# Performance work log

Measured on AMD Instinct MI355X. Metric: run time of the kernel, lower is better.

The kernel has to match this reference:

```python
import jax, jax.numpy as jnp
import numpy as np

B, S = 1, 2048
H, KV, D = 32, 8, 128          # query heads, kv heads, head_size
G = H // KV                     # num_queries_per_kv (GQA group size)
SCALE = 1.0 / float(np.sqrt(D))


def setup_inputs() -> dict:
    key = jax.random.key(0)
    k1, k2, k3 = jax.random.split(key, 3)
    slopes = jnp.asarray(2.0 ** (-8.0 * np.arange(1, H + 1) / H), dtype=jnp.float32)
    return {
        "query": jax.random.normal(k1, (B, S, H * D), dtype=jnp.float32),
        "key": jax.random.normal(k2, (B, S, KV * D), dtype=jnp.float32),
        "value": jax.random.normal(k3, (B, S, KV * D), dtype=jnp.float32),
        "alibi_slopes": slopes,
    }


def reference(query, key, value, alibi_slopes):
    b, s, _ = query.shape
    # [B,S,H*D] -> [B,KV,G,S,D] (GQA unflatten of query heads into kv groups)
    q = query.reshape(b, s, KV, G, D).transpose(0, 2, 3, 1, 4)
    k = key.reshape(b, s, KV, D).transpose(0, 2, 1, 3)      # [B,KV,S,D]
    v = value.reshape(b, s, KV, D).transpose(0, 2, 1, 3)    # [B,KV,S,D]

    # _make_alibi_bias: bias[i,j] = (j - i) * slope_h, then unflatten heads to (KV, G)
    pos = jnp.arange(s)
    rel = (pos[None, :] - pos[:, None]).astype(query.dtype)         # [S,S]
    bias = alibi_slopes[:, None, None] * rel                        # [H,S,S]
    causal = jnp.where(pos[None, :] > pos[:, None], -jnp.inf, 0.0).astype(query.dtype)
    bias = (bias + causal).reshape(KV, G, s, s)                     # [KV,G,S,S]

    # scaled QK^T + bias, softmax, AV (non-fused prompt_attention path)
    scores = jnp.einsum('bkgsd,bktd->bkgst', q * SCALE, k) + bias   # [B,KV,G,S,S]
    probs = jax.nn.softmax(scores, axis=-1)
    out = jnp.einsum('bkgst,bktd->bkgsd', probs, v)                 # [B,KV,G,S,D]
    # flatten (KV,G) -> H and back to [B,S,H*D]
    return out.transpose(0, 3, 1, 2, 4).reshape(b, s, H * D)
```

## Files before the change

kernel.cpp:

```cpp
#include <hip/hip_runtime.h>
#include <hip/hip_bf16.h>

#define S_LEN 2048
#define NHEADS 32
#define NKV 8
#define HD 128
#define QK_SCALE 0.08838834764831845f
#define LOG2E 1.4426950408889634f
#define QK_SCALE2 (QK_SCALE * LOG2E)
#define DTHR 11.5416f

#define BQ 64
#define BK 32
#define NQT (S_LEN / BQ)
#define QSTR (NHEADS * HD)
#define KSTR (NKV * HD)

#define K_STRIDE 136
#define VT_STRIDE 40
#define P_STRIDE 40

typedef __attribute__((ext_vector_type(8))) short bf16x8;
typedef __attribute__((ext_vector_type(4))) float f32x4;
typedef __attribute__((ext_vector_type(4))) unsigned u32x4;
typedef __attribute__((ext_vector_type(2))) unsigned u32x2;

__device__ inline unsigned cvt_pk_bf16(float lo, float hi) {
    unsigned r;
    asm("v_cvt_pk_bf16_f32 %0, %1, %2" : "=v"(r) : "v"(lo), "v"(hi));
    return r;
}
__device__ inline bf16x8 as_bf16x8(u32x4 v) {
    union { u32x4 u; bf16x8 b; } c; c.u = v; return c.b;
}

__global__ __launch_bounds__(256) void prep_k(const float* __restrict__ K,
                                              short* __restrict__ Kbf) {
    int g = blockIdx.x * 256 + threadIdx.x;
    int chunk = g & 15, kvh = (g >> 4) & 7, s = g >> 7;
    const float* in = K + (size_t)s * KSTR + kvh * HD + chunk * 8;
    f32x4 a = *(const f32x4*)in;
    f32x4 b = *(const f32x4*)(in + 4);
    u32x4 t;
    t[0] = cvt_pk_bf16(a[0], a[1]); t[1] = cvt_pk_bf16(a[2], a[3]);
    t[2] = cvt_pk_bf16(b[0], b[1]); t[3] = cvt_pk_bf16(b[2], b[3]);
    *(u32x4*)(Kbf + ((size_t)kvh * S_LEN + s) * HD + chunk * 8) = t;
}

__global__ __launch_bounds__(256) void prep_v(const float* __restrict__ V,
                                              short* __restrict__ Vtb) {
    __shared__ short Ts[64][72];
    int b = blockIdx.x;
    int sb = b & 31, db = (b >> 5) & 1, kvh = b >> 6;
    int t = threadIdx.x, r = t >> 2, c0 = (t & 3) * 16;

    const float* in = V + (size_t)(sb * 64 + r) * KSTR + kvh * HD + db * 64 + c0;
    f32x4 a0 = *(const f32x4*)in,        a1 = *(const f32x4*)(in + 4);
    f32x4 a2 = *(const f32x4*)(in + 8),  a3 = *(const f32x4*)(in + 12);
    u32x4 t0;
    t0[0] = cvt_pk_bf16(a0[0], a0[1]); t0[1] = cvt_pk_bf16(a0[2], a0[3]);
    t0[2] = cvt_pk_bf16(a1[0], a1[1]); t0[3] = cvt_pk_bf16(a1[2], a1[3]);
    *(u32x4*)&Ts[r][c0] = t0;
    t0[0] = cvt_pk_bf16(a2[0], a2[1]); t0[1] = cvt_pk_bf16(a2[2], a2[3]);
    t0[2] = cvt_pk_bf16(a3[0], a3[1]); t0[3] = cvt_pk_bf16(a3[2], a3[3]);
    *(u32x4*)&Ts[r][c0 + 8] = t0;
    __syncthreads();

    alignas(16) short tmp[16];
    #pragma unroll
    for (int j = 0; j < 16; ++j) tmp[j] = Ts[c0 + j][r];
    short* dst = Vtb + ((size_t)(kvh * HD + db * 64 + r)) * S_LEN + sb * 64 + c0;
    *(u32x4*)dst       = *(u32x4*)&tmp[0];
    *(u32x4*)(dst + 8) = *(u32x4*)&tmp[8];
}

__global__ __launch_bounds__(256) void attn_fwd(
    const float* __restrict__ Q, const short* __restrict__ Kbf,
    const short* __restrict__ Vtb, const float* __restrict__ SL,
    float* __restrict__ O)
{
    const int bx   = blockIdx.x;
    const int h    = bx & (NHEADS - 1);
    const int qt   = (NQT - 1) - (bx >> 5);
    const int kvh  = h >> 2;
    const float slope  = SL[h];
    const float slope2 = slope * LOG2E;

    const int tid  = threadIdx.x;
    const int lane = tid & 63;
    const int w    = tid >> 6;
    const int l16  = lane & 15;
    const int lq   = lane >> 4;

    __shared__ short Ks[2][BK * K_STRIDE];
    __shared__ short VTs[2][HD * VT_STRIDE];
    __shared__ short Ps[4][16 * P_STRIDE];

    const int qrow0 = qt * BQ + w * 16;
    const int q     = qrow0 + l16;

    bf16x8 qf[4];
    {
        const float* qp = Q + (size_t)q * QSTR + h * HD + lq * 8;
        #pragma unroll
        for (int d0 = 0; d0 < 4; ++d0) {
            f32x4 a = *(const f32x4*)(qp + d0 * 32);
            f32x4 b = *(const f32x4*)(qp + d0 * 32 + 4);
            u32x4 t;
            t[0] = cvt_pk_bf16(a[0] * QK_SCALE2, a[1] * QK_SCALE2);
            t[1] = cvt_pk_bf16(a[2] * QK_SCALE2, a[3] * QK_SCALE2);
            t[2] = cvt_pk_bf16(b[0] * QK_SCALE2, b[1] * QK_SCALE2);
            t[3] = cvt_pk_bf16(b[2] * QK_SCALE2, b[3] * QK_SCALE2);
            qf[d0] = as_bf16x8(t);
        }
    }
    bf16x8 onesf;
    #pragma unroll
    for (int j = 0; j < 8; ++j) onesf[j] = (short)0x3f80;

    f32x4 acc[8];
    #pragma unroll
    for (int t = 0; t < 8; ++t) acc[t] = (f32x4){0.f, 0.f, 0.f, 0.f};
    f32x4 sums = (f32x4){0.f, 0.f, 0.f, 0.f};
    float m_ = -1e30f;

    const int kv_end = qt * BQ + BQ;
    int kb_start = 0;
    {
        float th = (float)(qt * BQ) - 31.0f - 45.0f / slope;
        int t = (int)floorf(th);
        kb_start = (t < 0) ? 0 : (((t >> 5) + 1) << 5);
    }

    const int sr  = tid >> 4, scc = tid & 15;
    const int vd  = tid & 127, vrb = (tid >> 7) * 8;
    const short* Kst = Kbf + (size_t)kvh * S_LEN * HD + scc * 8;
    const short* Vst = Vtb + (size_t)(kvh * HD + vd) * S_LEN;

    u32x4 kreg[2], vreg[2];

    auto load_regs = [&](int kb) {
        #pragma unroll
        for (int s = 0; s < 2; ++s)
            kreg[s] = *(const u32x4*)(Kst + (size_t)(kb + sr + s * 16) * HD);
        #pragma unroll
        for (int s = 0; s < 2; ++s)
            vreg[s] = *(const u32x4*)(Vst + kb + vrb + s * 16);
    };

    auto store_tile = [&](int b) {
        #pragma unroll
        for (int s = 0; s < 2; ++s)
            *(u32x4*)&Ks[b][(sr + s * 16) * K_STRIDE + scc * 8] = kreg[s];
        #pragma unroll
        for (int s = 0; s < 2; ++s)
            *(u32x4*)&VTs[b][vd * VT_STRIDE + vrb + s * 16] = vreg[s];
    };

    load_regs(kb_start);
    store_tile(0);
    int cur = 0;

    for (int kb = kb_start; kb < kv_end; kb += BK) {
        asm volatile("s_waitcnt lgkmcnt(0)\n\ts_barrier" ::: "memory");

        const bool has_next = (kb + BK) < kv_end;
        if (has_next) load_regs(kb + BK);

        const bool live = (kb <= qrow0 + 15) &&
                          (slope * (float)(qrow0 - kb - 31) < 45.0f);
        if (live) {
            const short* Kc = &Ks[cur][0];
            const short* Vc = &VTs[cur][0];

            f32x4 sc0 = (f32x4){0.f,0.f,0.f,0.f};
            f32x4 sc1 = (f32x4){0.f,0.f,0.f,0.f};
            #pragma unroll
            for (int d0 = 0; d0 < 4; ++d0) {
                bf16x8 kf0 = *(const bf16x8*)&Kc[l16 * K_STRIDE + d0 * 32 + lq * 8];
                bf16x8 kf1 = *(const bf16x8*)&Kc[(16 + l16) * K_STRIDE + d0 * 32 + lq * 8];
                sc0 = __builtin_amdgcn_mfma_f32_16x16x32_bf16(kf0, qf[d0], sc0, 0, 0, 0);
                sc1 = __builtin_amdgcn_mfma_f32_16x16x32_bf16(kf1, qf[d0], sc1, 0, 0, 0);
            }

            const int kq0 = kb + 4 * lq - q;
            float s[8];
            #pragma unroll
            for (int i = 0; i < 4; ++i) {
                int d0i = kq0 + i, d1i = kq0 + 16 + i;
                float b0 = __builtin_fmaf(slope2, (float)d0i, sc0[i]);
                float b1 = __builtin_fmaf(slope2, (float)d1i, sc1[i]);
                s[i]     = (d0i > 0) ? -1e30f : b0;
                s[i + 4] = (d1i > 0) ? -1e30f : b1;
            }

            float lm = fmaxf(fmaxf(fmaxf(s[0], s[1]), fmaxf(s[2], s[3])),
                             fmaxf(fmaxf(s[4], s[5]), fmaxf(s[6], s[7])));
            if (__any(lm > m_ + DTHR)) {
                float rm = lm;
                rm = fmaxf(rm, __shfl_xor(rm, 16));
                rm = fmaxf(rm, __shfl_xor(rm, 32));
                if (rm > m_ + DTHR) {
                    float alpha = exp2f(m_ - rm);
                    m_ = rm;
                    sums[0] *= alpha; sums[1] *= alpha;
                    sums[2] *= alpha; sums[3] *= alpha;
                    #pragma unroll
                    for (int t = 0; t < 8; ++t) {
                        acc[t][0] *= alpha; acc[t][1] *= alpha;
                        acc[t][2] *= alpha; acc[t][3] *= alpha;
                    }
                }
            }

            float p[8];
            #pragma unroll
            for (int j = 0; j < 8; ++j) p[j] = exp2f(s[j] - m_);

            u32x2 pa, pb;
            pa[0] = cvt_pk_bf16(p[0], p[1]); pa[1] = cvt_pk_bf16(p[2], p[3]);
            pb[0] = cvt_pk_bf16(p[4], p[5]); pb[1] = cvt_pk_bf16(p[6], p[7]);

            short* PsW = &Ps[w][0];
            *(u32x2*)&PsW[l16 * P_STRIDE + 4 * lq]      = pa;
            *(u32x2*)&PsW[l16 * P_STRIDE + 16 + 4 * lq] = pb;
            asm volatile("s_waitcnt lgkmcnt(0)" ::: "memory");
            bf16x8 pf = *(const bf16x8*)&PsW[l16 * P_STRIDE + lq * 8];

            sums = __builtin_amdgcn_mfma_f32_16x16x32_bf16(onesf, pf, sums, 0, 0, 0);

            #pragma unroll
            for (int nt = 0; nt < 8; ++nt) {
                bf16x8 vf = *(const bf16x8*)&Vc[(nt * 16 + l16) * VT_STRIDE + lq * 8];
                acc[nt] = __builtin_amdgcn_mfma_f32_16x16x32_bf16(vf, pf, acc[nt], 0, 0, 0);
            }
        }

        if (has_next) store_tile(cur ^ 1);
        cur ^= 1;
    }

    {
        float rl = 1.0f / sums[0];
        float* op = O + (size_t)q * QSTR + h * HD + 4 * lq;
        #pragma unroll
        for (int nt = 0; nt < 8; ++nt) {
            f32x4 o = acc[nt];
            o[0] *= rl; o[1] *= rl; o[2] *= rl; o[3] *= rl;
            *(f32x4*)(op + nt * 16) = o;
        }
    }
}

extern "C" void kernel_launch(void* const* d_in, const int* in_sizes, int n_in,
                              void* d_out, int out_size, void* d_ws, size_t ws_size,
                              hipStream_t stream) {
    const float* Q  = (const float*)d_in[0];
    const float* K  = (const float*)d_in[1];
    const float* V  = (const float*)d_in[2];
    const float* SL = (const float*)d_in[3];
    float* O = (float*)d_out;

    short* Kbf = (short*)d_ws;
    short* Vtb = (short*)d_ws + (size_t)NKV * S_LEN * HD;

    prep_k<<<dim3(1024), dim3(256), 0, stream>>>(K, Kbf);
    prep_v<<<dim3(512),  dim3(256), 0, stream>>>(V, Vtb);
    attn_fwd<<<dim3(NQT * NHEADS), dim3(256), 0, stream>>>(Q, Kbf, Vtb, SL, O);
}
```

Measured before the change: 90.64 us.

## Deepen K/V prefetch to two tiles ahead with ping-pong register slots

Restructures the KV loop into a two-step unrolled ping-pong pipeline. Two register slot sets hold the global loads for tiles t+1 and t+2 while tile t is computed from shared memory. Each shared store happens right after the barrier and before compute, rather than at the end of the iteration. The goal is to hide more global-memory latency behind MFMA work. The cost is about 32 extra VGPRs for the second slot, which may reduce occupancy.

```diff
diff --git a/kernel.cpp b/kernel.cpp
--- a/kernel.cpp
+++ b/kernel.cpp
@@ -131,113 +131,122 @@
         int t = (int)floorf(th);
         kb_start = (t < 0) ? 0 : (((t >> 5) + 1) << 5);
     }
+    const int Ntiles = (kv_end - kb_start) >> 5;
 
     const int sr  = tid >> 4, scc = tid & 15;
     const int vd  = tid & 127, vrb = (tid >> 7) * 8;
     const short* Kst = Kbf + (size_t)kvh * S_LEN * HD + scc * 8;
     const short* Vst = Vtb + (size_t)(kvh * HD + vd) * S_LEN;
 
-    u32x4 kreg[2], vreg[2];
-
-    auto load_regs = [&](int kb) {
-        #pragma unroll
-        for (int s = 0; s < 2; ++s)
-            kreg[s] = *(const u32x4*)(Kst + (size_t)(kb + sr + s * 16) * HD);
-        #pragma unroll
-        for (int s = 0; s < 2; ++s)
-            vreg[s] = *(const u32x4*)(Vst + kb + vrb + s * 16);
+    u32x4 kA[2], vA[2], kB[2], vB[2];
+
+    auto load_slot = [&](u32x4 (&kk)[2], u32x4 (&vv)[2], int kb) {
+        #pragma unroll
+        for (int s = 0; s < 2; ++s)
+            kk[s] = *(const u32x4*)(Kst + (size_t)(kb + sr + s * 16) * HD);
+        #pragma unroll
+        for (int s = 0; s < 2; ++s)
+            vv[s] = *(const u32x4*)(Vst + kb + vrb + s * 16);
     };
-
-    auto store_tile = [&](int b) {
-        #pragma unroll
-        for (int s = 0; s < 2; ++s)
-            *(u32x4*)&Ks[b][(sr + s * 16) * K_STRIDE + scc * 8] = kreg[s];
-        #pragma unroll
-        for (int s = 0; s < 2; ++s)
-            *(u32x4*)&VTs[b][vd * VT_STRIDE + vrb + s * 16] = vreg[s];
+    auto store_slot = [&](int b, u32x4 (&kk)[2], u32x4 (&vv)[2]) {
+        #pragma unroll
+        for (int s = 0; s < 2; ++s)
+            *(u32x4*)&Ks[b][(sr + s * 16) * K_STRIDE + scc * 8] = kk[s];
+        #pragma unroll
+        for (int s = 0; s < 2; ++s)
+            *(u32x4*)&VTs[b][vd * VT_STRIDE + vrb + s * 16] = vv[s];
     };
 
-    load_regs(kb_start);
-    store_tile(0);
-    int cur = 0;
-
-    for (int kb = kb_start; kb < kv_end; kb += BK) {
-        asm volatile("s_waitcnt lgkmcnt(0)\n\ts_barrier" ::: "memory");
-
-        const bool has_next = (kb + BK) < kv_end;
-        if (has_next) load_regs(kb + BK);
-
+    auto compute_tile = [&](int kb, int cb) {
         const bool live = (kb <= qrow0 + 15) &&
                           (slope * (float)(qrow0 - kb - 31) < 45.0f);
-        if (live) {
-            const short* Kc = &Ks[cur][0];
-            const short* Vc = &VTs[cur][0];
-
-            f32x4 sc0 = (f32x4){0.f,0.f,0.f,0.f};
-            f32x4 sc1 = (f32x4){0.f,0.f,0.f,0.f};
-            #pragma unroll
-            for (int d0 = 0; d0 < 4; ++d0) {
-                bf16x8 kf0 = *(const bf16x8*)&Kc[l16 * K_STRIDE + d0 * 32 + lq * 8];
-                bf16x8 kf1 = *(const bf16x8*)&Kc[(16 + l16) * K_STRIDE + d0 * 32 + lq * 8];
-                sc0 = __builtin_amdgcn_mfma_f32_16x16x32_bf16(kf0, qf[d0], sc0, 0, 0, 0);
-                sc1 = __builtin_amdgcn_mfma_f32_16x16x32_bf16(kf1, qf[d0], sc1, 0, 0, 0);
-            }
-
-            const int kq0 = kb + 4 * lq - q;
-            float s[8];
-            #pragma unroll
-            for (int i = 0; i < 4; ++i) {
-                int d0i = kq0 + i, d1i = kq0 + 16 + i;
-                float b0 = __builtin_fmaf(slope2, (float)d0i, sc0[i]);
-                float b1 = __builtin_fmaf(slope2, (float)d1i, sc1[i]);
-                s[i]     = (d0i > 0) ? -1e30f : b0;
-                s[i + 4] = (d1i > 0) ? -1e30f : b1;
-            }
-
-            float lm = fmaxf(fmaxf(fmaxf(s[0], s[1]), fmaxf(s[2], s[3])),
-                             fmaxf(fmaxf(s[4], s[5]), fmaxf(s[6], s[7])));
-            if (__any(lm > m_ + DTHR)) {
-                float rm = lm;
-                rm = fmaxf(rm, __shfl_xor(rm, 16));
-                rm = fmaxf(rm, __shfl_xor(rm, 32));
-                if (rm > m_ + DTHR) {
-                    float alpha = exp2f(m_ - rm);
-                    m_ = rm;
-                    sums[0] *= alpha; sums[1] *= alpha;
-                    sums[2] *= alpha; sums[3] *= alpha;
-                    #pragma unroll
-                    for (int t = 0; t < 8; ++t) {
-                        acc[t][0] *= alpha; acc[t][1] *= alpha;
-                        acc[t][2] *= alpha; acc[t][3] *= alpha;
-                    }
+        if (!live) return;
+        const short* Kc = &Ks[cb][0];
+        const short* Vc = &VTs[cb][0];
+
+        f32x4 sc0 = (f32x4){0.f,0.f,0.f,0.f};
+        f32x4 sc1 = (f32x4){0.f,0.f,0.f,0.f};
+        #pragma unroll
+        for (int d0 = 0; d0 < 4; ++d0) {
+            bf16x8 kf0 = *(const bf16x8*)&Kc[l16 * K_STRIDE + d0 * 32 + lq * 8];
+            bf16x8 kf1 = *(const bf16x8*)&Kc[(16 + l16) * K_STRIDE + d0 * 32 + lq * 8];
+            sc0 = __builtin_amdgcn_mfma_f32_16x16x32_bf16(kf0, qf[d0], sc0, 0, 0, 0);
+            sc1 = __builtin_amdgcn_mfma_f32_16x16x32_bf16(kf1, qf[d0], sc1, 0, 0, 0);
+        }
+
+        const int kq0 = kb + 4 * lq - q;
+        float s[8];
+        #pragma unroll
+        for (int i = 0; i < 4; ++i) {
+            int d0i = kq0 + i, d1i = kq0 + 16 + i;
+            float b0 = __builtin_fmaf(slope2, (float)d0i, sc0[i]);
+            float b1 = __builtin_fmaf(slope2, (float)d1i, sc1[i]);
+            s[i]     = (d0i > 0) ? -1e30f : b0;
+            s[i + 4] = (d1i > 0) ? -1e30f : b1;
+        }
+
+        float lm = fmaxf(fmaxf(fmaxf(s[0], s[1]), fmaxf(s[2], s[3])),
+                         fmaxf(fmaxf(s[4], s[5]), fmaxf(s[6], s[7])));
+        if (__any(lm > m_ + DTHR)) {
+            float rm = lm;
+            rm = fmaxf(rm, __shfl_xor(rm, 16));
+            rm = fmaxf(rm, __shfl_xor(rm, 32));
+            if (rm > m_ + DTHR) {
+                float alpha = exp2f(m_ - rm);
+                m_ = rm;
+                sums[0] *= alpha; sums[1] *= alpha;
+                sums[2] *= alpha; sums[3] *= alpha;
+                #pragma unroll
+                for (int t = 0; t < 8; ++t) {
+                    acc[t][0] *= alpha; acc[t][1] *= alpha;
+                    acc[t][2] *= alpha; acc[t][3] *= alpha;
                 }
             }
-
-            float p[8];
-            #pragma unroll
-            for (int j = 0; j < 8; ++j) p[j] = exp2f(s[j] - m_);
-
-            u32x2 pa, pb;
-            pa[0] = cvt_pk_bf16(p[0], p[1]); pa[1] = cvt_pk_bf16(p[2], p[3]);
-            pb[0] = cvt_pk_bf16(p[4], p[5]); pb[1] = cvt_pk_bf16(p[6], p[7]);
-
-            short* PsW = &Ps[w][0];
-            *(u32x2*)&PsW[l16 * P_STRIDE + 4 * lq]      = pa;
-            *(u32x2*)&PsW[l16 * P_STRIDE + 16 + 4 * lq] = pb;
-            asm volatile("s_waitcnt lgkmcnt(0)" ::: "memory");
-            bf16x8 pf = *(const bf16x8*)&PsW[l16 * P_STRIDE + lq * 8];
-
-            sums = __builtin_amdgcn_mfma_f32_16x16x32_bf16(onesf, pf, sums, 0, 0, 0);
-
-            #pragma unroll
-            for (int nt = 0; nt < 8; ++nt) {
-                bf16x8 vf = *(const bf16x8*)&Vc[(nt * 16 + l16) * VT_STRIDE + lq * 8];
-                acc[nt] = __builtin_amdgcn_mfma_f32_16x16x32_bf16(vf, pf, acc[nt], 0, 0, 0);
-            }
-        }
-
-        if (has_next) store_tile(cur ^ 1);
-        cur ^= 1;
+        }
+
+        float p[8];
+        #pragma unroll
+        for (int j = 0; j < 8; ++j) p[j] = exp2f(s[j] - m_);
+
+        u32x2 pa, pb;
+        pa[0] = cvt_pk_bf16(p[0], p[1]); pa[1] = cvt_pk_bf16(p[2], p[3]);
+        pb[0] = cvt_pk_bf16(p[4], p[5]); pb[1] = cvt_pk_bf16(p[6], p[7]);
+
+        short* PsW = &Ps[w][0];
+        *(u32x2*)&PsW[l16 * P_STRIDE + 4 * lq]      = pa;
+        *(u32x2*)&PsW[l16 * P_STRIDE + 16 + 4 * lq] = pb;
+        asm volatile("s_waitcnt lgkmcnt(0)" ::: "memory");
+        bf16x8 pf = *(const bf16x8*)&PsW[l16 * P_STRIDE + lq * 8];
+
+        sums = __builtin_amdgcn_mfma_f32_16x16x32_bf16(onesf, pf, sums, 0, 0, 0);
+
+        #pragma unroll
+        for (int nt = 0; nt < 8; ++nt) {
+            bf16x8 vf = *(const bf16x8*)&Vc[(nt * 16 + l16) * VT_STRIDE + lq * 8];
+            acc[nt] = __builtin_amdgcn_mfma_f32_16x16x32_bf16(vf, pf, acc[nt], 0, 0, 0);
+        }
+    };
+
+    load_slot(kA, vA, kb_start);
+    store_slot(0, kA, vA);
+    if (Ntiles > 1) load_slot(kB, vB, kb_start + 32);
+    if (Ntiles > 2) load_slot(kA, vA, kb_start + 64);
+
+    int t = 0;
+    for (; t + 2 <= Ntiles; t += 2) {
+        asm volatile("s_waitcnt lgkmcnt(0)\n\ts_barrier" ::: "memory");
+        store_slot(1, kB, vB);
+        if (t + 3 < Ntiles) load_slot(kB, vB, kb_start + (t + 3) * 32);
+        compute_tile(kb_start + t * 32, 0);
+
+        asm volatile("s_waitcnt lgkmcnt(0)\n\ts_barrier" ::: "memory");
+        if (t + 2 < Ntiles) store_slot(0, kA, vA);
+        if (t + 4 < Ntiles) load_slot(kA, vA, kb_start + (t + 4) * 32);
+        compute_tile(kb_start + (t + 1) * 32, 1);
+    }
+    if (t < Ntiles) {
+        asm volatile("s_waitcnt lgkmcnt(0)\n\ts_barrier" ::: "memory");
+        compute_tile(kb_start + t * 32, 0);
     }
 
     {
```

Result: slower. 105.4 us, median of 2 (+16.3%).

## Double query rows per wave to reuse K/V LDS tiles across two sub-tiles

Applied to the files above, without the earlier changes.

Raises the query tile from 64 to 128 rows so each wave handles two 16-row sub-tiles (A and B), each with its own softmax state and accumulators. K and V fragments read from shared memory now feed MFMAs for both sub-tiles, and each K/V tile is staged once for twice as many queries. This halves the grid and roughly doubles accumulator register pressure, which may lower occupancy. It also coarsens the load balance across causal tiles.

```diff
diff --git a/kernel.cpp b/kernel.cpp
--- a/kernel.cpp
+++ b/kernel.cpp
@@ -10,7 +10,7 @@
 #define QK_SCALE2 (QK_SCALE * LOG2E)
 #define DTHR 11.5416f
 
-#define BQ 64
+#define BQ 128
 #define BK 32
 #define NQT (S_LEN / BQ)
 #define QSTR (NHEADS * HD)
@@ -94,14 +94,16 @@
 
     __shared__ short Ks[2][BK * K_STRIDE];
     __shared__ short VTs[2][HD * VT_STRIDE];
-    __shared__ short Ps[4][16 * P_STRIDE];
-
-    const int qrow0 = qt * BQ + w * 16;
-    const int q     = qrow0 + l16;
-
-    bf16x8 qf[4];
-    {
-        const float* qp = Q + (size_t)q * QSTR + h * HD + lq * 8;
+    __shared__ short Ps[4][32 * P_STRIDE];
+
+    const int qrow0 = qt * BQ + w * 32;
+    const int qA    = qrow0 + l16;
+    const int qB    = qA + 16;
+
+    bf16x8 qfA[4], qfB[4];
+    #pragma unroll
+    for (int st = 0; st < 2; ++st) {
+        const float* qp = Q + (size_t)(st ? qB : qA) * QSTR + h * HD + lq * 8;
         #pragma unroll
         for (int d0 = 0; d0 < 4; ++d0) {
             f32x4 a = *(const f32x4*)(qp + d0 * 32);
@@ -111,18 +113,21 @@
             t[1] = cvt_pk_bf16(a[2] * QK_SCALE2, a[3] * QK_SCALE2);
             t[2] = cvt_pk_bf16(b[0] * QK_SCALE2, b[1] * QK_SCALE2);
             t[3] = cvt_pk_bf16(b[2] * QK_SCALE2, b[3] * QK_SCALE2);
-            qf[d0] = as_bf16x8(t);
+            if (st) qfB[d0] = as_bf16x8(t); else qfA[d0] = as_bf16x8(t);
         }
     }
     bf16x8 onesf;
     #pragma unroll
     for (int j = 0; j < 8; ++j) onesf[j] = (short)0x3f80;
 
-    f32x4 acc[8];
+    f32x4 accA[8], accB[8];
     #pragma unroll
-    for (int t = 0; t < 8; ++t) acc[t] = (f32x4){0.f, 0.f, 0.f, 0.f};
-    f32x4 sums = (f32x4){0.f, 0.f, 0.f, 0.f};
-    float m_ = -1e30f;
+    for (int t = 0; t < 8; ++t) {
+        accA[t] = (f32x4){0.f, 0.f, 0.f, 0.f};
+        accB[t] = (f32x4){0.f, 0.f, 0.f, 0.f};
+    }
+    f32x4 sumsA = (f32x4){0.f,0.f,0.f,0.f}, sumsB = (f32x4){0.f,0.f,0.f,0.f};
+    float mA = -1e30f, mB = -1e30f;
 
     const int kv_end = qt * BQ + BQ;
     int kb_start = 0;
@@ -147,7 +152,6 @@
         for (int s = 0; s < 2; ++s)
             vreg[s] = *(const u32x4*)(Vst + kb + vrb + s * 16);
     };
-
     auto store_tile = [&](int b) {
         #pragma unroll
         for (int s = 0; s < 2; ++s)
@@ -167,72 +171,126 @@
         const bool has_next = (kb + BK) < kv_end;
         if (has_next) load_regs(kb + BK);
 
-        const bool live = (kb <= qrow0 + 15) &&
-                          (slope * (float)(qrow0 - kb - 31) < 45.0f);
-        if (live) {
+        const bool liveA = (kb <= qrow0 + 15) &&
+                           (slope * (float)(qrow0 - kb - 31) < 45.0f);
+        const bool liveB = (kb <= qrow0 + 31) &&
+                           (slope * (float)(qrow0 + 16 - kb - 31) < 45.0f);
+
+        if (liveA || liveB) {
             const short* Kc = &Ks[cur][0];
             const short* Vc = &VTs[cur][0];
 
-            f32x4 sc0 = (f32x4){0.f,0.f,0.f,0.f};
-            f32x4 sc1 = (f32x4){0.f,0.f,0.f,0.f};
+            f32x4 sA0 = (f32x4){0.f,0.f,0.f,0.f}, sA1 = (f32x4){0.f,0.f,0.f,0.f};
+            f32x4 sB0 = (f32x4){0.f,0.f,0.f,0.f}, sB1 = (f32x4){0.f,0.f,0.f,0.f};
             #pragma unroll
             for (int d0 = 0; d0 < 4; ++d0) {
                 bf16x8 kf0 = *(const bf16x8*)&Kc[l16 * K_STRIDE + d0 * 32 + lq * 8];
                 bf16x8 kf1 = *(const bf16x8*)&Kc[(16 + l16) * K_STRIDE + d0 * 32 + lq * 8];
-                sc0 = __builtin_amdgcn_mfma_f32_16x16x32_bf16(kf0, qf[d0], sc0, 0, 0, 0);
-                sc1 = __builtin_amdgcn_mfma_f32_16x16x32_bf16(kf1, qf[d0], sc1, 0, 0, 0);
+                if (liveA) {
+                    sA0 = __builtin_amdgcn_mfma_f32_16x16x32_bf16(kf0, qfA[d0], sA0, 0, 0, 0);
+                    sA1 = __builtin_amdgcn_mfma_f32_16x16x32_bf16(kf1, qfA[d0], sA1, 0, 0, 0);
+                }
+                if (liveB) {
+                    sB0 = __builtin_amdgcn_mfma_f32_16x16x32_bf16(kf0, qfB[d0], sB0, 0, 0, 0);
+                    sB1 = __builtin_amdgcn_mfma_f32_16x16x32_bf16(kf1, qfB[d0], sB1, 0, 0, 0);
+                }
             }
 
-            const int kq0 = kb + 4 * lq - q;
-            float s[8];
-            #pragma unroll
-            for (int i = 0; i < 4; ++i) {
-                int d0i = kq0 + i, d1i = kq0 + 16 + i;
-                float b0 = __builtin_fmaf(slope2, (float)d0i, sc0[i]);
-                float b1 = __builtin_fmaf(slope2, (float)d1i, sc1[i]);
-                s[i]     = (d0i > 0) ? -1e30f : b0;
-                s[i + 4] = (d1i > 0) ? -1e30f : b1;
+            short* PsW = &Ps[w][0];
+            bool pvA = false, pvB = false;
+
+            if (liveA) {
+                const int kq0 = kb + 4 * lq - qA;
+                float s[8];
+                #pragma unroll
+                for (int i = 0; i < 4; ++i) {
+                    int d0i = kq0 + i, d1i = kq0 + 16 + i;
+                    float b0 = __builtin_fmaf(slope2, (float)d0i, sA0[i]);
+                    float b1 = __builtin_fmaf(slope2, (float)d1i, sA1[i]);
+                    s[i]     = (d0i > 0) ? -1e30f : b0;
+                    s[i + 4] = (d1i > 0) ? -1e30f : b1;
+                }
+                float lm = fmaxf(fmaxf(fmaxf(s[0], s[1]), fmaxf(s[2], s[3])),
+                                 fmaxf(fmaxf(s[4], s[5]), fmaxf(s[6], s[7])));
+                if (__any(lm > mA + DTHR)) {
+                    float rm = lm;
+                    rm = fmaxf(rm, __shfl_xor(rm, 16));
+                    rm = fmaxf(rm, __shfl_xor(rm, 32));
+                    if (rm > mA + DTHR) {
+                        float alpha = exp2f(mA - rm);
+                        mA = rm;
+                        sumsA[0] *= alpha; sumsA[1] *= alpha;
+                        sumsA[2] *= alpha; sumsA[3] *= alpha;
+                        #pragma unroll
+                        for (int t = 0; t < 8; ++t) {
+                            accA[t][0] *= alpha; accA[t][1] *= alpha;
+                            accA[t][2] *= alpha; accA[t][3] *= alpha;
+                        }
+                    }
+                }
+                float p[8];
+                #pragma unroll
+                for (int j = 0; j < 8; ++j) p[j] = exp2f(s[j] - mA);
+                u32x2 pa, pb;
+                pa[0] = cvt_pk_bf16(p[0], p[1]); pa[1] = cvt_pk_bf16(p[2], p[3]);
+                pb[0] = cvt_pk_bf16(p[4], p[5]); pb[1] = cvt_pk_bf16(p[6], p[7]);
+                *(u32x2*)&PsW[l16 * P_STRIDE + 4 * lq]      = pa;
+                *(u32x2*)&PsW[l16 * P_STRIDE + 16 + 4 * lq] = pb;
+                pvA = true;
             }
-
-            float lm = fmaxf(fmaxf(fmaxf(s[0], s[1]), fmaxf(s[2], s[3])),
-                             fmaxf(fmaxf(s[4], s[5]), fmaxf(s[6], s[7])));
-            if (__any(lm > m_ + DTHR)) {
-                float rm = lm;
-                rm = fmaxf(rm, __shfl_xor(rm, 16));
-                rm = fmaxf(rm, __shfl_xor(rm, 32));
-                if (rm > m_ + DTHR) {
-                    float alpha = exp2f(m_ - rm);
-                    m_ = rm;
-                    sums[0] *= alpha; sums[1] *= alpha;
-                    sums[2] *= alpha; sums[3] *= alpha;
-                    #pragma unroll
-                    for (int t = 0; t < 8; ++t) {
-                        acc[t][0] *= alpha; acc[t][1] *= alpha;
-                        acc[t][2] *= alpha; acc[t][3] *= alpha;
+            if (liveB) {
+                const int kq0 = kb + 4 * lq - qB;
+                float s[8];
+                #pragma unroll
+                for (int i = 0; i < 4; ++i) {
+                    int d0i = kq0 + i, d1i = kq0 + 16 + i;
+                    float b0 = __builtin_fmaf(slope2, (float)d0i, sB0[i]);
+                    float b1 = __builtin_fmaf(slope2, (float)d1i, sB1[i]);
+                    s[i]     = (d0i > 0) ? -1e30f : b0;
+                    s[i + 4] = (d1i > 0) ? -1e30f : b1;
+                }
+                float lm = fmaxf(fmaxf(fmaxf(s[0], s[1]), fmaxf(s[2], s[3])),
+                                 fmaxf(fmaxf(s[4], s[5]), fmaxf(s[6], s[7])));
+                if (__any(lm > mB + DTHR)) {
+                    float rm = lm;
+                    rm = fmaxf(rm, __shfl_xor(rm, 16));
+                    rm = fmaxf(rm, __shfl_xor(rm, 32));
+                    if (rm > mB + DTHR) {
+                        float alpha = exp2f(mB - rm);
+                        mB = rm;
+                        sumsB[0] *= alpha; sumsB[1] *= alpha;
+                        sumsB[2] *= alpha; sumsB[3] *= alpha;
+                        #pragma unroll
+                        for (int t = 0; t < 8; ++t) {
+                            accB[t][0] *= alpha; accB[t][1] *= alpha;
+                            accB[t][2] *= alpha; accB[t][3] *= alpha;
+                        }
                     }
                 }
+                float p[8];
+                #pragma unroll
+                for (int j = 0; j < 8; ++j) p[j] = exp2f(s[j] - mB);
+                u32x2 pa, pb;
+                pa[0] = cvt_pk_bf16(p[0], p[1]); pa[1] = cvt_pk_bf16(p[2], p[3]);
+                pb[0] = cvt_pk_bf16(p[4], p[5]); pb[1] = cvt_pk_bf16(p[6], p[7]);
+                *(u32x2*)&PsW[(16 + l16) * P_STRIDE + 4 * lq]      = pa;
+                *(u32x2*)&PsW[(16 + l16) * P_STRIDE + 16 + 4 * lq] = pb;
+                pvB = true;
             }
 
-            float p[8];
-            #pragma unroll
-            for (int j = 0; j < 8; ++j) p[j] = exp2f(s[j] - m_);
-
-            u32x2 pa, pb;
-            pa[0] = cvt_pk_bf16(p[0], p[1]); pa[1] = cvt_pk_bf16(p[2], p[3]);
-            pb[0] = cvt_pk_bf16(p[4], p[5]); pb[1] = cvt_pk_bf16(p[6], p[7]);
-
-            short* PsW = &Ps[w][0];
-            *(u32x2*)&PsW[l16 * P_STRIDE + 4 * lq]      = pa;
-            *(u32x2*)&PsW[l16 * P_STRIDE + 16 + 4 * lq] = pb;
             asm volatile("s_waitcnt lgkmcnt(0)" ::: "memory");
-            bf16x8 pf = *(const bf16x8*)&PsW[l16 * P_STRIDE + lq * 8];
-
-            sums = __builtin_amdgcn_mfma_f32_16x16x32_bf16(onesf, pf, sums, 0, 0, 0);
+            bf16x8 pfA, pfB;
+            if (pvA) pfA = *(const bf16x8*)&PsW[l16 * P_STRIDE + lq * 8];
+            if (pvB) pfB = *(const bf16x8*)&PsW[(16 + l16) * P_STRIDE + lq * 8];
+
+            if (pvA) sumsA = __builtin_amdgcn_mfma_f32_16x16x32_bf16(onesf, pfA, sumsA, 0, 0, 0);
+            if (pvB) sumsB = __builtin_amdgcn_mfma_f32_16x16x32_bf16(onesf, pfB, sumsB, 0, 0, 0);
 
             #pragma unroll
             for (int nt = 0; nt < 8; ++nt) {
                 bf16x8 vf = *(const bf16x8*)&Vc[(nt * 16 + l16) * VT_STRIDE + lq * 8];
-                acc[nt] = __builtin_amdgcn_mfma_f32_16x16x32_bf16(vf, pf, acc[nt], 0, 0, 0);
+                if (pvA) accA[nt] = __builtin_amdgcn_mfma_f32_16x16x32_bf16(vf, pfA, accA[nt], 0, 0, 0);
+                if (pvB) accB[nt] = __builtin_amdgcn_mfma_f32_16x16x32_bf16(vf, pfB, accB[nt], 0, 0, 0);
             }
         }
 
@@ -241,13 +299,21 @@
     }
 
     {
-        float rl = 1.0f / sums[0];
-        float* op = O + (size_t)q * QSTR + h * HD + 4 * lq;
+        float rlA = 1.0f / sumsA[0];
+        float* opA = O + (size_t)qA * QSTR + h * HD + 4 * lq;
         #pragma unroll
         for (int nt = 0; nt < 8; ++nt) {
-            f32x4 o = acc[nt];
-            o[0] *= rl; o[1] *= rl; o[2] *= rl; o[3] *= rl;
-            *(f32x4*)(op + nt * 16) = o;
+            f32x4 o = accA[nt];
+            o[0] *= rlA; o[1] *= rlA; o[2] *= rlA; o[3] *= rlA;
+            *(f32x4*)(opA + nt * 16) = o;
+        }
+        float rlB = 1.0f / sumsB[0];
+        float* opB = O + (size_t)qB * QSTR + h * HD + 4 * lq;
+        #pragma unroll
+        for (int nt = 0; nt < 8; ++nt) {
+            f32x4 o = accB[nt];
+            o[0] *= rlB; o[1] *= rlB; o[2] *= rlB; o[3] *= rlB;
+            *(f32x4*)(opB + nt * 16) = o;
         }
     }
 }
```

After: 198.8 us. 119% more time.
